# Performance work log

Hardware: AMD Instinct MI355X
Metric: run time of the kernel (lower is better)

Reference implementation:

```python
import jax, jax.numpy as jnp
import numpy as np

IMG_DIM = 256
AUD_DIM = 256
N_HEADS = 8


def _linear_params(key, fan_in, fan_out):
    k1, k2 = jax.random.split(key)
    lim = 1.0 / np.sqrt(fan_in)
    W = jax.random.uniform(k1, (fan_in, fan_out), minval=-lim, maxval=lim, dtype=jnp.float32)
    b = jax.random.uniform(k2, (fan_out,), minval=-lim, maxval=lim, dtype=jnp.float32)
    return W, b


def setup_inputs() -> dict:
    key = jax.random.key(0)
    ks = jax.random.split(key, 16)
    B, Nv, Na = 16, 1024, 512
    inp = {
        "image_feat": jax.random.normal(ks[0], (B, Nv, IMG_DIM), dtype=jnp.float32),
        "audio_feat": jax.random.normal(ks[1], (B, Na, AUD_DIM), dtype=jnp.float32),
    }
    inp["Wq_i"], inp["bq_i"] = _linear_params(ks[2], IMG_DIM, IMG_DIM)
    inp["Wk_i"], inp["bk_i"] = _linear_params(ks[3], IMG_DIM, IMG_DIM)
    inp["Wv_i"], inp["bv_i"] = _linear_params(ks[4], IMG_DIM, IMG_DIM)
    inp["Wo_i"], inp["bo_i"] = _linear_params(ks[5], AUD_DIM, IMG_DIM)  # out_proj_image
    inp["Wq_a"], inp["bq_a"] = _linear_params(ks[6], AUD_DIM, AUD_DIM)
    inp["Wk_a"], inp["bk_a"] = _linear_params(ks[7], AUD_DIM, AUD_DIM)
    inp["Wv_a"], inp["bv_a"] = _linear_params(ks[8], AUD_DIM, AUD_DIM)
    inp["Wo_a"], inp["bo_a"] = _linear_params(ks[9], IMG_DIM, AUD_DIM)  # out_proj_audio
    inp["Wc1_i"], inp["bc1_i"] = _linear_params(ks[10], IMG_DIM + 2, IMG_DIM)
    inp["Wc2_i"], inp["bc2_i"] = _linear_params(ks[11], IMG_DIM, N_HEADS)
    inp["Wc1_a"], inp["bc1_a"] = _linear_params(ks[12], AUD_DIM + 2, AUD_DIM)
    inp["Wc2_a"], inp["bc2_a"] = _linear_params(ks[13], AUD_DIM, N_HEADS)
    inp["Wg_i"], inp["bg_i"] = _linear_params(ks[14], IMG_DIM, IMG_DIM)
    inp["Wg_a"], inp["bg_a"] = _linear_params(ks[15], AUD_DIM, AUD_DIM)
    return inp


def _heads(x, W, b, H):
    # x: [B, N, C] -> [B, H, N, C//H]
    B, N, _ = x.shape
    y = x @ W + b
    return y.reshape(B, N, H, -1).transpose(0, 2, 1, 3)


def _fwd(image_feat, audio_feat,
         Wq_i, bq_i, Wk_i, bk_i, Wv_i, bv_i, Wo_i, bo_i,
         Wq_a, bq_a, Wk_a, bk_a, Wv_a, bv_a, Wo_a, bo_a,
         Wc1_i, bc1_i, Wc2_i, bc2_i, Wc1_a, bc1_a, Wc2_a, bc2_a,
         Wg_i, bg_i, Wg_a, bg_a):
    H = N_HEADS
    B, Nv, Ci = image_feat.shape
    _, Na, Ca = audio_feat.shape
    scale_img = (Ci // H) ** (-0.5)
    scale_aud = (Ca // H) ** (-0.5)

    tp_img = image_feat.mean(axis=1)  # [B, Ci]
    tp_aud = audio_feat.mean(axis=1)  # [B, Ca]
    spatial_cond = jnp.linalg.norm(image_feat, axis=-1).mean(axis=1, keepdims=True)  # [B,1]
    time_cond = jnp.linalg.norm(audio_feat, axis=-1).mean(axis=1, keepdims=True)     # [B,1]

    # --- audio queries attend over image keys/values ---
    Q_a = _heads(audio_feat, Wq_a, bq_a, H)   # [B,H,Na,d]
    K_i = _heads(image_feat, Wk_i, bk_i, H)   # [B,H,Nv,d]
    V_i = _heads(image_feat, Wv_i, bv_i, H)   # [B,H,Nv,d]
    cond_aud = jnp.concatenate([tp_aud, spatial_cond, time_cond], axis=-1)  # [B,Ca+2]
    bias_a = (jax.nn.relu(cond_aud @ Wc1_a + bc1_a) @ Wc2_a + bc2_a)        # [B,H]
    logits_a = jnp.einsum('bhqd,bhkd->bhqk', Q_a, K_i) * scale_aud + bias_a[:, :, None, None]
    attn_a = jax.nn.softmax(logits_a, axis=-1)
    fused_a = jnp.einsum('bhqk,bhkd->bhqd', attn_a, V_i)  # [B,H,Na,d]
    fused_a = fused_a.transpose(0, 2, 1, 3).reshape(B, Na, Ci)
    fused_a = fused_a @ Wo_a + bo_a                        # [B,Na,Ca]
    gate_a = jax.nn.sigmoid(tp_aud @ Wg_a + bg_a)[:, None, :]
    audio_out = gate_a * fused_a + (1.0 - gate_a) * audio_feat

    # --- image queries attend over UPDATED audio keys/values ---
    Q_i = _heads(image_feat, Wq_i, bq_i, H)   # [B,H,Nv,d]
    K_a = _heads(audio_out, Wk_a, bk_a, H)    # [B,H,Na,d]
    V_a = _heads(audio_out, Wv_a, bv_a, H)    # [B,H,Na,d]
    cond_img = jnp.concatenate([tp_img, spatial_cond, time_cond], axis=-1)  # [B,Ci+2]
    bias_i = (jax.nn.relu(cond_img @ Wc1_i + bc1_i) @ Wc2_i + bc2_i)        # [B,H]
    logits_i = jnp.einsum('bhqd,bhkd->bhqk', Q_i, K_a) * scale_img + bias_i[:, :, None, None]
    attn_i = jax.nn.softmax(logits_i, axis=-1)
    fused_i = jnp.einsum('bhqk,bhkd->bhqd', attn_i, V_a)  # [B,H,Nv,d]
    fused_i = fused_i.transpose(0, 2, 1, 3).reshape(B, Nv, Ca)
    fused_i = fused_i @ Wo_i + bo_i                        # [B,Nv,Ci]
    gate_i = jax.nn.sigmoid(tp_img @ Wg_i + bg_i)[:, None, :]
    image_out = gate_i * fused_i + (1.0 - gate_i) * image_feat

    return image_out, audio_out


def reference(image_feat, audio_feat,
              Wq_i, bq_i, Wk_i, bk_i, Wv_i, bv_i, Wo_i, bo_i,
              Wq_a, bq_a, Wk_a, bk_a, Wv_a, bv_a, Wo_a, bo_a,
              Wc1_i, bc1_i, Wc2_i, bc2_i, Wc1_a, bc1_a, Wc2_a, bc2_a,
              Wg_i, bg_i, Wg_a, bg_a):
    return _fwd(image_feat, audio_feat,
                Wq_i, bq_i, Wk_i, bk_i, Wv_i, bv_i, Wo_i, bo_i,
                Wq_a, bq_a, Wk_a, bk_a, Wv_a, bv_a, Wo_a, bo_a,
                Wc1_i, bc1_i, Wc2_i, bc2_i, Wc1_a, bc1_a, Wc2_a, bc2_a,
                Wg_i, bg_i, Wg_a, bg_a)
```

## Files before the change

### kernel.cpp

```cpp
#include <hip/hip_runtime.h>

#define C 256

typedef short s16x8 __attribute__((ext_vector_type(8)));
typedef float f32x4 __attribute__((ext_vector_type(4)));

#if __has_builtin(__builtin_amdgcn_exp2f)
#define EXP2F __builtin_amdgcn_exp2f
#else
#define EXP2F exp2f
#endif

__device__ __forceinline__ unsigned short f2b(float f) {
    unsigned u = __float_as_uint(f);
    unsigned r = (u + 0x7fffu + ((u >> 16) & 1u)) >> 16;
    return (unsigned short)r;
}

__device__ __forceinline__ unsigned pack2(float a, float b) {
    return __builtin_amdgcn_perm(__float_as_uint(b) + 0x8000u,
                                 __float_as_uint(a) + 0x8000u, 0x07060302u);
}

struct WPtrs { const float* src[8]; unsigned short* dst[8]; };

__device__ __forceinline__ void cast_mean_body(
    const float* __restrict__ x, unsigned short* __restrict__ y, float* __restrict__ part,
    int N, int nseg, int b, int seg, int tid) {
    __shared__ float red[4][C];
    int cg = tid & 63, rg = tid >> 6;
    int iters = nseg >> 2;
    const float* xp = x + ((size_t)b * N + (size_t)seg * nseg + rg) * C + cg * 4;
    unsigned short* yp = y + ((size_t)b * N + (size_t)seg * nseg + rg) * C + cg * 4;
    float s0 = 0.f, s1 = 0.f, s2 = 0.f, s3 = 0.f;
    for (int i = 0; i < iters; ++i) {
        float4 v = *(const float4*)(xp + (size_t)i * 4 * C);
        s0 += v.x; s1 += v.y; s2 += v.z; s3 += v.w;
        ushort4 o; o.x = f2b(v.x); o.y = f2b(v.y); o.z = f2b(v.z); o.w = f2b(v.w);
        *(ushort4*)(yp + (size_t)i * 4 * C) = o;
    }
    float4 s4 = {s0, s1, s2, s3};
    *(float4*)&red[rg][cg * 4] = s4;
    __syncthreads();
    float s = red[0][tid] + red[1][tid] + red[2][tid] + red[3][tid];
    part[(b * 8 + seg) * C + tid] = s;
}

__global__ void prep_kernel(const float* __restrict__ img, const float* __restrict__ aud,
                            unsigned short* __restrict__ R1, unsigned short* __restrict__ R4,
                            float* __restrict__ partI, float* __restrict__ partA, WPtrs wp) {
    int x = blockIdx.x, tid = threadIdx.x;
    if (x < 128) {
        cast_mean_body(img, R1, partI, 1024, 128, x >> 3, x & 7, tid);
    } else if (x < 256) {
        int id = x - 128;
        cast_mean_body(aud, R4, partA, 512, 64, id >> 3, id & 7, tid);
    } else {
        int id = x - 256;
        const float* W = wp.src[id >> 2];
        unsigned short* Wt = wp.dst[id >> 2];
        int n = (id & 3) * 64 + (tid & 63);
        int k0 = (tid >> 6) * 64;
#pragma unroll
        for (int kk = 0; kk < 64; kk += 4) {
            float a0 = W[(size_t)(k0 + kk + 0) * C + n];
            float a1 = W[(size_t)(k0 + kk + 1) * C + n];
            float a2 = W[(size_t)(k0 + kk + 2) * C + n];
            float a3 = W[(size_t)(k0 + kk + 3) * C + n];
            ushort4 o; o.x = f2b(a0); o.y = f2b(a1); o.z = f2b(a2); o.w = f2b(a3);
            *(ushort4*)(Wt + (size_t)n * C + k0 + kk) = o;
        }
    }
}

struct GDesc {
    const unsigned short* A;
    const unsigned short* Bt;
    const float* bias;
    unsigned short* Yh;
    int N;
    int start;
    int lnb;
    int bias_on_m;
    float oscale;
};
struct GArgs {
    GDesc d[4];
    int off1, off2, off3;
    int gemm_total;
    const float* partI; const float* partA;
    const float* WgI; const float* WgA;
    const float* bgI; const float* bgA;
    float* gI; float* gA;
    float invNv, invNa;
};

__global__ __launch_bounds__(256, 2) void gemm_multi(GArgs ga) {
    __shared__ unsigned short sA[128 * 40];
    __shared__ unsigned short sB[64 * 40];
    const int bid = blockIdx.x;
    const int tid = threadIdx.x;

    if (bid >= ga.gemm_total) {
        float* t = (float*)sA;
        int id = bid - ga.gemm_total;
        int b = id >> 1, which = id & 1;
        const float* part = which ? ga.partA : ga.partI;
        const float* Wg = which ? ga.WgA : ga.WgI;
        const float* bg = which ? ga.bgA : ga.bgI;
        float* g = which ? ga.gA : ga.gI;
        float invN = which ? ga.invNa : ga.invNv;
        float s = 0.f;
#pragma unroll
        for (int j = 0; j < 8; ++j) s += part[(b * 8 + j) * C + tid];
        t[tid] = s * invN;
        __syncthreads();
        float acc = bg[tid];
#pragma unroll 8
        for (int k = 0; k < C; ++k) acc += t[k] * Wg[k * C + tid];
        g[b * C + tid] = 1.f / (1.f + __expf(-acc));
        return;
    }

    const int j = (bid >= ga.off1) + (bid >= ga.off2) + (bid >= ga.off3);
    const GDesc d = ga.d[j];
    const int local = bid - d.start;
    const int bn = (local & ((1 << d.lnb) - 1)) * 64;
    const int bm = (local >> d.lnb) * 128;

    const int wave = tid >> 6, lane = tid & 63;
    const int quad = lane >> 4, l16 = lane & 15;
    const int ar0 = tid >> 2, ac0 = tid & 3;
    const int ar1 = (tid + 256) >> 2;
    const int br = tid >> 2, bc = tid & 3;

    f32x4 acc[2][4];
#pragma unroll
    for (int i = 0; i < 2; ++i)
#pragma unroll
        for (int k = 0; k < 4; ++k) acc[i][k] = (f32x4){0.f, 0.f, 0.f, 0.f};

    uint4 pa0 = *(const uint4*)(d.A + (size_t)(bm + ar0) * 256 + ac0 * 8);
    uint4 pa1 = *(const uint4*)(d.A + (size_t)(bm + ar1) * 256 + ac0 * 8);
    uint4 pb  = *(const uint4*)(d.Bt + (size_t)(bn + br) * 256 + bc * 8);

    for (int k0 = 0; k0 < 256; k0 += 32) {
        __syncthreads();
        *(uint4*)(sA + ar0 * 40 + ac0 * 8) = pa0;
        *(uint4*)(sA + ar1 * 40 + ac0 * 8) = pa1;
        *(uint4*)(sB + br * 40 + bc * 8) = pb;
        if (k0 < 224) {
            pa0 = *(const uint4*)(d.A + (size_t)(bm + ar0) * 256 + k0 + 32 + ac0 * 8);
            pa1 = *(const uint4*)(d.A + (size_t)(bm + ar1) * 256 + k0 + 32 + ac0 * 8);
            pb  = *(const uint4*)(d.Bt + (size_t)(bn + br) * 256 + k0 + 32 + bc * 8);
        }
        __syncthreads();
        s16x8 af[2], bf[4];
#pragma unroll
        for (int mt = 0; mt < 2; ++mt)
            af[mt] = *(const s16x8*)(sA + (wave * 32 + mt * 16 + l16) * 40 + quad * 8);
#pragma unroll
        for (int nt = 0; nt < 4; ++nt)
            bf[nt] = *(const s16x8*)(sB + (nt * 16 + l16) * 40 + quad * 8);
#pragma unroll
        for (int mt = 0; mt < 2; ++mt)
#pragma unroll
            for (int nt = 0; nt < 4; ++nt)
                acc[mt][nt] = __builtin_amdgcn_mfma_f32_16x16x32_bf16(af[mt], bf[nt], acc[mt][nt], 0, 0, 0);
    }

#pragma unroll
    for (int mt = 0; mt < 2; ++mt) {
#pragma unroll
        for (int nt = 0; nt < 4; ++nt) {
            int n = bn + nt * 16 + l16;
            float bias_n = d.bias_on_m ? 0.f : d.bias[n];
#pragma unroll
            for (int r = 0; r < 4; ++r) {
                int m = bm + wave * 32 + mt * 16 + quad * 4 + r;
                float y = acc[mt][nt][r] + (d.bias_on_m ? d.bias[m] : bias_n);
                d.Yh[(size_t)m * d.N + n] = f2b(y * d.oscale);
            }
        }
    }
}

template <bool STORE_BF16>
__global__ __launch_bounds__(256, 2) void gemm_out(
    const unsigned short* __restrict__ A, const unsigned short* __restrict__ Bt,
    const float* __restrict__ bias, float* __restrict__ Yf, unsigned short* __restrict__ Yh,
    int M, const float* __restrict__ gate, const float* __restrict__ resid, int rows_per_b) {
    __shared__ unsigned short sA[128 * 40];
    __shared__ unsigned short sB[64 * 40];
    const int tid = threadIdx.x;
    const int wave = tid >> 6, lane = tid & 63;
    const int quad = lane >> 4, l16 = lane & 15;
    const int bm = blockIdx.y * 128, bn = blockIdx.x * 64;
    const int ar0 = tid >> 2, ac0 = tid & 3;
    const int ar1 = (tid + 256) >> 2;
    const int br = tid >> 2, bc = tid & 3;

    f32x4 acc[2][4];
#pragma unroll
    for (int i = 0; i < 2; ++i)
#pragma unroll
        for (int k = 0; k < 4; ++k) acc[i][k] = (f32x4){0.f, 0.f, 0.f, 0.f};

    uint4 pa0 = *(const uint4*)(A + (size_t)(bm + ar0) * 256 + ac0 * 8);
    uint4 pa1 = *(const uint4*)(A + (size_t)(bm + ar1) * 256 + ac0 * 8);
    uint4 pb  = *(const uint4*)(Bt + (size_t)(bn + br) * 256 + bc * 8);

    for (int k0 = 0; k0 < 256; k0 += 32) {
        __syncthreads();
        *(uint4*)(sA + ar0 * 40 + ac0 * 8) = pa0;
        *(uint4*)(sA + ar1 * 40 + ac0 * 8) = pa1;
        *(uint4*)(sB + br * 40 + bc * 8) = pb;
        if (k0 < 224) {
            pa0 = *(const uint4*)(A + (size_t)(bm + ar0) * 256 + k0 + 32 + ac0 * 8);
            pa1 = *(const uint4*)(A + (size_t)(bm + ar1) * 256 + k0 + 32 + ac0 * 8);
            pb  = *(const uint4*)(Bt + (size_t)(bn + br) * 256 + k0 + 32 + bc * 8);
        }
        __syncthreads();
        s16x8 af[2], bf[4];
#pragma unroll
        for (int mt = 0; mt < 2; ++mt)
            af[mt] = *(const s16x8*)(sA + (wave * 32 + mt * 16 + l16) * 40 + quad * 8);
#pragma unroll
        for (int nt = 0; nt < 4; ++nt)
            bf[nt] = *(const s16x8*)(sB + (nt * 16 + l16) * 40 + quad * 8);
#pragma unroll
        for (int mt = 0; mt < 2; ++mt)
#pragma unroll
            for (int nt = 0; nt < 4; ++nt)
                acc[mt][nt] = __builtin_amdgcn_mfma_f32_16x16x32_bf16(af[mt], bf[nt], acc[mt][nt], 0, 0, 0);
    }

    const int b = bm / rows_per_b;
#pragma unroll
    for (int mt = 0; mt < 2; ++mt) {
#pragma unroll
        for (int nt = 0; nt < 4; ++nt) {
            int n = bn + nt * 16 + l16;
            float bias_n = bias[n];
            float g = gate[b * C + n];
#pragma unroll
            for (int r = 0; r < 4; ++r) {
                int m = bm + wave * 32 + mt * 16 + quad * 4 + r;
                float y = acc[mt][nt][r] + bias_n;
                float rv = resid[(size_t)m * C + n];
                y = g * y + (1.f - g) * rv;
                Yf[(size_t)m * C + n] = y;
                if (STORE_BF16) Yh[(size_t)m * C + n] = f2b(y);
            }
        }
    }
}

__global__ __launch_bounds__(256) void attn_mfma(
    const unsigned short* __restrict__ Q, const unsigned short* __restrict__ K,
    const unsigned short* __restrict__ Vt, unsigned short* __restrict__ O,
    int Nq, int Nk, int vtStride) {
    __shared__ unsigned short sP[4][2][16 * 40];
    const int tid = threadIdx.x;
    const int wave = tid >> 6, lane = tid & 63;
    const int quad = lane >> 4, l16 = lane & 15;
    const int b = blockIdx.z, h = blockIdx.y;
    const int q0 = blockIdx.x * 128 + wave * 32;

    s16x8 qf[2];
    qf[0] = *(const s16x8*)(Q + ((size_t)b * Nq + q0 + l16) * 256 + h * 32 + quad * 8);
    qf[1] = *(const s16x8*)(Q + ((size_t)b * Nq + q0 + 16 + l16) * 256 + h * 32 + quad * 8);
    f32x4 oacc[2][2];
#pragma unroll
    for (int i = 0; i < 2; ++i)
#pragma unroll
        for (int k = 0; k < 2; ++k) oacc[i][k] = (f32x4){0.f, 0.f, 0.f, 0.f};
    float rs[2] = {0.f, 0.f};

    const unsigned short* Kf = K + ((size_t)b * Nk + l16) * 256 + h * 32 + quad * 8;
    const unsigned short* Vf0 = Vt + (size_t)(h * 32 + l16) * vtStride + (size_t)b * Nk + quad * 8;
    const unsigned short* Vf1 = Vf0 + (size_t)16 * vtStride;

    s16x8 kr[4], vr[4];
#pragma unroll
    for (int t = 0; t < 4; ++t) kr[t] = *(const s16x8*)(Kf + (size_t)t * 16 * 256);
    vr[0] = *(const s16x8*)(Vf0);
    vr[1] = *(const s16x8*)(Vf0 + 32);
    vr[2] = *(const s16x8*)(Vf1);
    vr[3] = *(const s16x8*)(Vf1 + 32);

    for (int k0 = 0; k0 < Nk; k0 += 64) {
        const int kp = (k0 + 64 < Nk) ? k0 + 64 : k0;
        s16x8 kn[4], vn[4];
#pragma unroll
        for (int t = 0; t < 4; ++t) kn[t] = *(const s16x8*)(Kf + (size_t)(kp + t * 16) * 256);
        vn[0] = *(const s16x8*)(Vf0 + kp);
        vn[1] = *(const s16x8*)(Vf0 + kp + 32);
        vn[2] = *(const s16x8*)(Vf1 + kp);
        vn[3] = *(const s16x8*)(Vf1 + kp + 32);

#pragma unroll
        for (int kg = 0; kg < 2; ++kg) {
#pragma unroll
            for (int q2 = 0; q2 < 2; ++q2) {
                unsigned short* p = &sP[wave][q2][0];
#pragma unroll
                for (int kt = 0; kt < 2; ++kt) {
                    f32x4 z = (f32x4){0.f, 0.f, 0.f, 0.f};
                    f32x4 st = __builtin_amdgcn_mfma_f32_16x16x32_bf16(kr[kg * 2 + kt], qf[q2], z, 0, 0, 0);
                    float p0 = EXP2F(st[0]), p1 = EXP2F(st[1]);
                    float p2 = EXP2F(st[2]), p3 = EXP2F(st[3]);
                    rs[q2] += (p0 + p1) + (p2 + p3);
                    uint2 pk;
                    pk.x = pack2(p0, p1);
                    pk.y = pack2(p2, p3);
                    *(uint2*)(p + l16 * 40 + kt * 16 + quad * 4) = pk;
                }
            }
#pragma unroll
            for (int q2 = 0; q2 < 2; ++q2) {
                s16x8 pf = *(const s16x8*)(&sP[wave][q2][0] + l16 * 40 + quad * 8);
                oacc[q2][0] = __builtin_amdgcn_mfma_f32_16x16x32_bf16(pf, vr[kg], oacc[q2][0], 0, 0, 0);
                oacc[q2][1] = __builtin_amdgcn_mfma_f32_16x16x32_bf16(pf, vr[2 + kg], oacc[q2][1], 0, 0, 0);
            }
        }
#pragma unroll
        for (int t = 0; t < 4; ++t) { kr[t] = kn[t]; vr[t] = vn[t]; }
    }

#pragma unroll
    for (int q2 = 0; q2 < 2; ++q2) {
        float r = rs[q2];
        r += __shfl_xor(r, 16, 64);
        r += __shfl_xor(r, 32, 64);
        float inv = 1.f / r;
#pragma unroll
        for (int rr = 0; rr < 4; ++rr) {
            float iq = __shfl(inv, quad * 4 + rr, 64);
#pragma unroll
            for (int dh = 0; dh < 2; ++dh)
                O[((size_t)b * Nq + q0 + q2 * 16 + quad * 4 + rr) * 256 + h * 32 + dh * 16 + l16] =
                    f2b(oacc[q2][dh][rr] * iq);
        }
    }
}

extern "C" void kernel_launch(void* const* d_in, const int* in_sizes, int n_in,
                              void* d_out, int out_size, void* d_ws, size_t ws_size,
                              hipStream_t stream) {
    (void)in_sizes; (void)n_in; (void)out_size; (void)ws_size;
    const float* img  = (const float*)d_in[0];
    const float* aud  = (const float*)d_in[1];
    const float* Wq_i = (const float*)d_in[2];  const float* bq_i = (const float*)d_in[3];
    const float* Wk_i = (const float*)d_in[4];  const float* bk_i = (const float*)d_in[5];
    const float* Wv_i = (const float*)d_in[6];  const float* bv_i = (const float*)d_in[7];
    const float* Wo_i = (const float*)d_in[8];  const float* bo_i = (const float*)d_in[9];
    const float* Wq_a = (const float*)d_in[10]; const float* bq_a = (const float*)d_in[11];
    const float* Wk_a = (const float*)d_in[12]; const float* bk_a = (const float*)d_in[13];
    const float* Wv_a = (const float*)d_in[14]; const float* bv_a = (const float*)d_in[15];
    const float* Wo_a = (const float*)d_in[16]; const float* bo_a = (const float*)d_in[17];
    const float* Wg_i = (const float*)d_in[26]; const float* bg_i = (const float*)d_in[27];
    const float* Wg_a = (const float*)d_in[28]; const float* bg_a = (const float*)d_in[29];

    const int B = 16, Nv = 1024, Na = 512;
    const int Mi = B * Nv, Ma = B * Na;
    const size_t MiC = (size_t)Mi * C;
    const size_t MaC = (size_t)Ma * C;

    float* out_img = (float*)d_out;
    float* out_aud = out_img + MiC;

    unsigned short* wsu = (unsigned short*)d_ws;
    unsigned short* R1 = wsu;
    unsigned short* R2 = R1 + MiC;
    unsigned short* R3 = R2 + MiC;
    unsigned short* R8 = R3 + MiC;
    unsigned short* R4 = R8 + MiC;
    unsigned short* R5 = R4 + MaC;
    unsigned short* R6 = R5 + MaC;
    unsigned short* R7 = R6 + MaC;
    unsigned short* wt = R7 + MaC;
    float* fws   = (float*)(wt + 8 * 65536);
    float* partI = fws;
    float* partA = partI + B * 8 * C;
    float* gI    = partA + B * 8 * C;
    float* gA    = gI + B * C;

    unsigned short* wtQa = wt + 0 * 65536;
    unsigned short* wtKi = wt + 1 * 65536;
    unsigned short* wtVi = wt + 2 * 65536;
    unsigned short* wtOa = wt + 3 * 65536;
    unsigned short* wtKa = wt + 4 * 65536;
    unsigned short* wtVa = wt + 5 * 65536;
    unsigned short* wtQi = wt + 6 * 65536;
    unsigned short* wtOi = wt + 7 * 65536;

    const float qs = 0.17677669529663687f * 1.4426950408889634f;
    dim3 blk(256);

    WPtrs wp;
    wp.src[0] = Wq_a; wp.dst[0] = wtQa;
    wp.src[1] = Wk_i; wp.dst[1] = wtKi;
    wp.src[2] = Wv_i; wp.dst[2] = wtVi;
    wp.src[3] = Wo_a; wp.dst[3] = wtOa;
    wp.src[4] = Wk_a; wp.dst[4] = wtKa;
    wp.src[5] = Wv_a; wp.dst[5] = wtVa;
    wp.src[6] = Wq_i; wp.dst[6] = wtQi;
    wp.src[7] = Wo_i; wp.dst[7] = wtOi;
    prep_kernel<<<288, blk, 0, stream>>>(img, aud, R1, R4, partI, partA, wp);

    GArgs g1 = {};
    g1.d[0] = {R4,   wtQa, bq_a, R5, 256,   0,    2, 0, qs };
    g1.d[1] = {R1,   wtKi, bk_i, R2, 256,   256,  2, 0, 1.f};
    g1.d[2] = {wtVi, R1,   bv_i, R3, 16384, 768,  8, 1, 1.f};
    g1.d[3] = {R1,   wtQi, bq_i, R8, 256,   1280, 2, 0, qs };
    g1.off1 = 256; g1.off2 = 768; g1.off3 = 1280; g1.gemm_total = 1792;
    g1.partI = partI; g1.partA = partA;
    g1.WgI = Wg_i; g1.WgA = Wg_a; g1.bgI = bg_i; g1.bgA = bg_a;
    g1.gI = gI; g1.gA = gA; g1.invNv = 1.f / Nv; g1.invNa = 1.f / Na;
    gemm_multi<<<1792 + 32, blk, 0, stream>>>(g1);

    attn_mfma<<<dim3(Na / 128, 8, B), blk, 0, stream>>>(R5, R2, R3, R6, Na, Nv, Mi);

    gemm_out<true><<<dim3(4, Ma / 128), blk, 0, stream>>>(R6, wtOa, bo_a, out_aud, R7, Ma, gA, aud, Na);

    GArgs g2 = {};
    g2.d[0] = {R7,   wtKa, bk_a, R5, 256,  0,   2, 0, 1.f};
    g2.d[1] = {wtVa, R7,   bv_a, R6, 8192, 256, 7, 1, 1.f};
    g2.off1 = 256; g2.off2 = 512; g2.off3 = 512; g2.gemm_total = 512;
    gemm_multi<<<512, blk, 0, stream>>>(g2);

    attn_mfma<<<dim3(Nv / 128, 8, B), blk, 0, stream>>>(R8, R5, R6, R2, Nv, Na, Ma);

    gemm_out<false><<<dim3(4, Mi / 128), blk, 0, stream>>>(R2, wtOi, bo_i, out_img, nullptr, Mi, gI, img, Nv);
}
```

Before: 280.2 us.

## Stage K/V tiles in shared memory and halve per-block query tile in attention

The attention kernel now loads each 64-key K and V^T tile cooperatively into LDS once per block, with register prefetch of the next tile, instead of every wave loading its own copies from global memory. Each wave handles 16 queries instead of 32, so the grid doubles and more blocks are launched, with launch bounds raised for occupancy. The cost is two __syncthreads per key tile and extra LDS traffic, plus half the reuse of K/V per wave.

```diff
diff --git a/kernel.cpp b/kernel.cpp
--- a/kernel.cpp
+++ b/kernel.cpp
@@ -256,92 +256,78 @@
     }
 }
 
-__global__ __launch_bounds__(256) void attn_mfma(
+__global__ __launch_bounds__(256, 8) void attn_mfma(
     const unsigned short* __restrict__ Q, const unsigned short* __restrict__ K,
     const unsigned short* __restrict__ Vt, unsigned short* __restrict__ O,
     int Nq, int Nk, int vtStride) {
-    __shared__ unsigned short sP[4][2][16 * 40];
+    __shared__ unsigned short sK[64 * 34];
+    __shared__ unsigned short sVt[32 * 66];
+    __shared__ unsigned short sP[4][16 * 70];
     const int tid = threadIdx.x;
     const int wave = tid >> 6, lane = tid & 63;
     const int quad = lane >> 4, l16 = lane & 15;
     const int b = blockIdx.z, h = blockIdx.y;
-    const int q0 = blockIdx.x * 128 + wave * 32;
-
-    s16x8 qf[2];
-    qf[0] = *(const s16x8*)(Q + ((size_t)b * Nq + q0 + l16) * 256 + h * 32 + quad * 8);
-    qf[1] = *(const s16x8*)(Q + ((size_t)b * Nq + q0 + 16 + l16) * 256 + h * 32 + quad * 8);
-    f32x4 oacc[2][2];
-#pragma unroll
-    for (int i = 0; i < 2; ++i)
-#pragma unroll
-        for (int k = 0; k < 2; ++k) oacc[i][k] = (f32x4){0.f, 0.f, 0.f, 0.f};
-    float rs[2] = {0.f, 0.f};
-
-    const unsigned short* Kf = K + ((size_t)b * Nk + l16) * 256 + h * 32 + quad * 8;
-    const unsigned short* Vf0 = Vt + (size_t)(h * 32 + l16) * vtStride + (size_t)b * Nk + quad * 8;
-    const unsigned short* Vf1 = Vf0 + (size_t)16 * vtStride;
-
-    s16x8 kr[4], vr[4];
-#pragma unroll
-    for (int t = 0; t < 4; ++t) kr[t] = *(const s16x8*)(Kf + (size_t)t * 16 * 256);
-    vr[0] = *(const s16x8*)(Vf0);
-    vr[1] = *(const s16x8*)(Vf0 + 32);
-    vr[2] = *(const s16x8*)(Vf1);
-    vr[3] = *(const s16x8*)(Vf1 + 32);
+    const int q0 = blockIdx.x * 64 + wave * 16;
+
+    s16x8 qf = *(const s16x8*)(Q + ((size_t)b * Nq + q0 + l16) * 256 + h * 32 + quad * 8);
+    f32x4 oacc[2];
+    oacc[0] = (f32x4){0.f, 0.f, 0.f, 0.f};
+    oacc[1] = (f32x4){0.f, 0.f, 0.f, 0.f};
+    float rs = 0.f;
+
+    const int kr = tid >> 2, kc = tid & 3;
+    const int vr = tid >> 3, vc = tid & 7;
+    const unsigned short* Kb = K + (size_t)b * Nk * 256 + h * 32;
+    const unsigned short* Vb = Vt + (size_t)(h * 32 + vr) * vtStride + (size_t)b * Nk;
+
+    uint4 kreg = *(const uint4*)(Kb + (size_t)kr * 256 + kc * 8);
+    uint4 vreg = *(const uint4*)(Vb + vc * 8);
 
     for (int k0 = 0; k0 < Nk; k0 += 64) {
-        const int kp = (k0 + 64 < Nk) ? k0 + 64 : k0;
-        s16x8 kn[4], vn[4];
-#pragma unroll
-        for (int t = 0; t < 4; ++t) kn[t] = *(const s16x8*)(Kf + (size_t)(kp + t * 16) * 256);
-        vn[0] = *(const s16x8*)(Vf0 + kp);
-        vn[1] = *(const s16x8*)(Vf0 + kp + 32);
-        vn[2] = *(const s16x8*)(Vf1 + kp);
-        vn[3] = *(const s16x8*)(Vf1 + kp + 32);
-
+        __syncthreads();
+        *(uint4*)(sK + kr * 34 + kc * 8) = kreg;
+        *(uint4*)(sVt + vr * 66 + vc * 8) = vreg;
+        if (k0 + 64 < Nk) {
+            kreg = *(const uint4*)(Kb + (size_t)(k0 + 64 + kr) * 256 + kc * 8);
+            vreg = *(const uint4*)(Vb + k0 + 64 + vc * 8);
+        }
+        __syncthreads();
+
+        unsigned short* p = &sP[wave][0];
+#pragma unroll
+        for (int t = 0; t < 4; ++t) {
+            s16x8 kf = *(const s16x8*)(sK + (t * 16 + l16) * 34 + quad * 8);
+            f32x4 z = (f32x4){0.f, 0.f, 0.f, 0.f};
+            f32x4 st = __builtin_amdgcn_mfma_f32_16x16x32_bf16(kf, qf, z, 0, 0, 0);
+            float p0 = EXP2F(st[0]), p1 = EXP2F(st[1]);
+            float p2 = EXP2F(st[2]), p3 = EXP2F(st[3]);
+            rs += (p0 + p1) + (p2 + p3);
+            uint2 pk;
+            pk.x = pack2(p0, p1);
+            pk.y = pack2(p2, p3);
+            *(uint2*)(p + l16 * 70 + t * 16 + quad * 4) = pk;
+        }
 #pragma unroll
         for (int kg = 0; kg < 2; ++kg) {
-#pragma unroll
-            for (int q2 = 0; q2 < 2; ++q2) {
-                unsigned short* p = &sP[wave][q2][0];
-#pragma unroll
-                for (int kt = 0; kt < 2; ++kt) {
-                    f32x4 z = (f32x4){0.f, 0.f, 0.f, 0.f};
-                    f32x4 st = __builtin_amdgcn_mfma_f32_16x16x32_bf16(kr[kg * 2 + kt], qf[q2], z, 0, 0, 0);
-                    float p0 = EXP2F(st[0]), p1 = EXP2F(st[1]);
-                    float p2 = EXP2F(st[2]), p3 = EXP2F(st[3]);
-                    rs[q2] += (p0 + p1) + (p2 + p3);
-                    uint2 pk;
-                    pk.x = pack2(p0, p1);
-                    pk.y = pack2(p2, p3);
-                    *(uint2*)(p + l16 * 40 + kt * 16 + quad * 4) = pk;
-                }
+            s16x8 pf = *(const s16x8*)(p + l16 * 70 + kg * 32 + quad * 8);
+#pragma unroll
+            for (int dh = 0; dh < 2; ++dh) {
+                s16x8 vf = *(const s16x8*)(sVt + (dh * 16 + l16) * 66 + kg * 32 + quad * 8);
+                oacc[dh] = __builtin_amdgcn_mfma_f32_16x16x32_bf16(pf, vf, oacc[dh], 0, 0, 0);
             }
-#pragma unroll
-            for (int q2 = 0; q2 < 2; ++q2) {
-                s16x8 pf = *(const s16x8*)(&sP[wave][q2][0] + l16 * 40 + quad * 8);
-                oacc[q2][0] = __builtin_amdgcn_mfma_f32_16x16x32_bf16(pf, vr[kg], oacc[q2][0], 0, 0, 0);
-                oacc[q2][1] = __builtin_amdgcn_mfma_f32_16x16x32_bf16(pf, vr[2 + kg], oacc[q2][1], 0, 0, 0);
-            }
-        }
-#pragma unroll
-        for (int t = 0; t < 4; ++t) { kr[t] = kn[t]; vr[t] = vn[t]; }
-    }
-
-#pragma unroll
-    for (int q2 = 0; q2 < 2; ++q2) {
-        float r = rs[q2];
-        r += __shfl_xor(r, 16, 64);
-        r += __shfl_xor(r, 32, 64);
-        float inv = 1.f / r;
-#pragma unroll
-        for (int rr = 0; rr < 4; ++rr) {
-            float iq = __shfl(inv, quad * 4 + rr, 64);
-#pragma unroll
-            for (int dh = 0; dh < 2; ++dh)
-                O[((size_t)b * Nq + q0 + q2 * 16 + quad * 4 + rr) * 256 + h * 32 + dh * 16 + l16] =
-                    f2b(oacc[q2][dh][rr] * iq);
-        }
+        }
+    }
+
+    rs += __shfl_xor(rs, 16, 64);
+    rs += __shfl_xor(rs, 32, 64);
+    float inv = 1.f / rs;
+#pragma unroll
+    for (int rr = 0; rr < 4; ++rr) {
+        float iq = __shfl(inv, quad * 4 + rr, 64);
+#pragma unroll
+        for (int dh = 0; dh < 2; ++dh)
+            O[((size_t)b * Nq + q0 + quad * 4 + rr) * 256 + h * 32 + dh * 16 + l16] =
+                f2b(oacc[dh][rr] * iq);
     }
 }
 
@@ -420,7 +406,7 @@
     g1.gI = gI; g1.gA = gA; g1.invNv = 1.f / Nv; g1.invNa = 1.f / Na;
     gemm_multi<<<1792 + 32, blk, 0, stream>>>(g1);
 
-    attn_mfma<<<dim3(Na / 128, 8, B), blk, 0, stream>>>(R5, R2, R3, R6, Na, Nv, Mi);
+    attn_mfma<<<dim3(Na / 64, 8, B), blk, 0, stream>>>(R5, R2, R3, R6, Na, Nv, Mi);
 
     gemm_out<true><<<dim3(4, Ma / 128), blk, 0, stream>>>(R6, wtOa, bo_a, out_aud, R7, Ma, gA, aud, Na);
 
@@ -430,7 +416,7 @@
     g2.off1 = 256; g2.off2 = 512; g2.off3 = 512; g2.gemm_total = 512;
     gemm_multi<<<512, blk, 0, stream>>>(g2);
 
-    attn_mfma<<<dim3(Nv / 128, 8, B), blk, 0, stream>>>(R8, R5, R6, R2, Nv, Na, Ma);
+    attn_mfma<<<dim3(Nv / 64, 8, B), blk, 0, stream>>>(R8, R5, R6, R2, Nv, Na, Ma);
 
     gemm_out<false><<<dim3(4, Mi / 128), blk, 0, stream>>>(R2, wtOi, bo_i, out_img, nullptr, Mi, gI, img, Nv);
 }
```

Result: slower. 321.2 us (+14.7%).
